# Optimization experiments

Hardware: AMD Instinct MI355X
Metric: run time of the kernel (lower is better)

The kernel has to match this reference:

```python
import jax, jax.numpy as jnp
import numpy as np
import math

B, S, HID = 2, 2048, 4096
H, HD = 32, HID // 32  # num_heads, head_dim


def setup_inputs() -> dict:
    key = jax.random.key(0)
    ks = jax.random.split(key, 7)
    hidden_states = jax.random.normal(ks[0], (B, S, HID), jnp.float32)
    residual = jax.random.normal(ks[1], (B, S, HID), jnp.float32)
    # BLOOM alibi: [B*H, 1, kv_len]; realistic slopes * positions
    slopes = jnp.asarray(2.0 ** (-8.0 * (np.arange(1, H + 1) / H)), jnp.float32)  # [H]
    alibi = (slopes[:, None] * jnp.arange(S, dtype=jnp.float32)[None, :])  # [H, S]
    alibi = jnp.broadcast_to(alibi[None], (B, H, S)).reshape(B * H, 1, S)
    # causal mask: True = masked (upper triangle)
    causal = ~jnp.tril(jnp.ones((S, S), bool))
    attention_mask = jnp.broadcast_to(causal[None, None], (B, 1, S, S))
    Wqkv = jax.random.normal(ks[2], (HID, 3 * HID), jnp.float32) * 0.02
    bqkv = jax.random.normal(ks[3], (3 * HID,), jnp.float32) * 0.02
    Wd = jax.random.normal(ks[4], (HID, HID), jnp.float32) * 0.02
    bd = jax.random.normal(ks[5], (HID,), jnp.float32) * 0.02
    return {"hidden_states": hidden_states, "residual": residual, "alibi": alibi,
            "attention_mask": attention_mask, "Wqkv": Wqkv, "bqkv": bqkv,
            "Wd": Wd, "bd": bd}


def reference(hidden_states, residual, alibi, attention_mask, Wqkv, bqkv, Wd, bd):
    b, s, _ = hidden_states.shape
    inv_norm = 1.0 / math.sqrt(HD)
    fused = hidden_states @ Wqkv + bqkv                       # [b,s,3*HID]
    fused = fused.reshape(b, s, H, 3, HD)
    q = jnp.transpose(fused[..., 0, :], (0, 2, 1, 3))         # [b,H,s,hd]
    k = jnp.transpose(fused[..., 1, :], (0, 2, 1, 3))
    v = jnp.transpose(fused[..., 2, :], (0, 2, 1, 3))
    # baddbmm: alibi + inv_norm * q @ k^T
    scores = jnp.einsum('bhqd,bhkd->bhqk', q, k) * inv_norm
    scores = scores + alibi.reshape(b, H, 1, s)               # broadcast over q
    neg = jnp.finfo(jnp.float32).min
    scores = jnp.where(attention_mask, neg, scores)
    probs = jax.nn.softmax(scores.astype(jnp.float32), axis=-1)
    ctx = jnp.einsum('bhqk,bhkd->bhqd', probs, v)             # [b,H,s,hd]
    ctx = jnp.transpose(ctx, (0, 2, 1, 3)).reshape(b, s, HID)
    out = ctx @ Wd + bd
    return residual + out
```

## Files before the change

### kernel.cpp

```cpp
#include <hip/hip_runtime.h>
#include <cstdint>
#include <cstddef>


typedef unsigned short u16;
typedef unsigned int u32;
typedef __bf16 bf16x8 __attribute__((ext_vector_type(8)));
typedef float f32x4 __attribute__((ext_vector_type(4)));
typedef u16 u16x4 __attribute__((ext_vector_type(4)));

#define LDS_AS(p) ((__attribute__((address_space(3))) u32*)(p))
#define GLB_AS(p) ((__attribute__((address_space(1))) u32*)(p))

__device__ __forceinline__ void load16(const void* g, void* l) {
  __builtin_amdgcn_global_load_lds(GLB_AS(g), LDS_AS(l), 16, 0, 0);
}

__device__ __forceinline__ u16 f2bf(float f) {
  union { float f; u32 u; } x; x.f = f;
  u32 r = x.u + 0x7fffu + ((x.u >> 16) & 1u);
  return (u16)(r >> 16);
}

__global__ __launch_bounds__(256) void cvt_bf16(const float* __restrict__ in,
                                                u16* __restrict__ out, int n) {
  int i = (blockIdx.x * 256 + threadIdx.x) * 4;
  if (i >= n) return;
  float4 v = *(const float4*)(in + i);
  u16x4 o = { f2bf(v.x), f2bf(v.y), f2bf(v.z), f2bf(v.w) };
  *(u16x4*)(out + i) = o;
}

__global__ __launch_bounds__(256) void cvt_transpose(const float* __restrict__ W,
                                                     u16* __restrict__ WT,
                                                     int K, int N) {
  __shared__ float tile[32][33];
  int n0 = blockIdx.x * 32, k0 = blockIdx.y * 32;
  int tx = threadIdx.x & 31, ty = threadIdx.x >> 5;
  for (int r = ty; r < 32; r += 8)
    tile[r][tx] = W[(size_t)(k0 + r) * N + n0 + tx];
  __syncthreads();
  for (int r = ty; r < 32; r += 8)
    WT[(size_t)(n0 + r) * K + k0 + tx] = f2bf(tile[tx][r]);
}

__global__ __launch_bounds__(256) void transpose_v(const u16* __restrict__ fused,
                                                   u16* __restrict__ vt) {
  __shared__ __align__(16) u16 tile[64][136];
  int st = blockIdx.x * 64, bh = blockIdx.y;
  int b = bh >> 5, h = bh & 31;
  int tx = threadIdx.x & 15, ty = threadIdx.x >> 4;
  for (int r = ty; r < 64; r += 16) {
    const u16* src = fused + (size_t)(b * 2048 + st + r) * 12288 + h * 384 + 256 + tx * 8;
    u16x4 a = *(const u16x4*)(src);
    u16x4 c = *(const u16x4*)(src + 4);
    *(u16x4*)&tile[r][tx * 8] = a;
    *(u16x4*)&tile[r][tx * 8 + 4] = c;
  }
  __syncthreads();
  for (int d = ty; d < 128; d += 16) {
    u16x4 o = { tile[tx * 4 + 0][d], tile[tx * 4 + 1][d],
                tile[tx * 4 + 2][d], tile[tx * 4 + 3][d] };
    *(u16x4*)(vt + ((size_t)bh * 128 + d) * 2048 + st + tx * 4) = o;
  }
}

template <int EPI>
__global__ __launch_bounds__(256) void gemm_bt(const u16* __restrict__ A,
                                               const u16* __restrict__ BT,
                                               const float* __restrict__ bias,
                                               const float* __restrict__ res,
                                               void* __restrict__ out,
                                               int M, int N, int K) {
  __shared__ __align__(16) u16 As[128 * 32];
  __shared__ __align__(16) u16 Bs[128 * 32];
  const int tid = threadIdx.x, wave = tid >> 6, lane = tid & 63;
  const int quad = lane >> 4, l16 = lane & 15;
  const int m0 = blockIdx.y * 128, n0 = blockIdx.x * 128;
  const int wm = (wave >> 1) * 64, wn = (wave & 1) * 64;

  const f32x4 fz = {0.f, 0.f, 0.f, 0.f};
  f32x4 acc[4][4];
  for (int i = 0; i < 4; ++i)
    for (int j = 0; j < 4; ++j) acc[i][j] = fz;

  const int i0 = wave * 2;
  const int t0 = i0 * 1024 + lane * 16;
  const int t1 = t0 + 1024;
  const int rA0 = t0 >> 6, cA0 = t0 & 63;
  const int rA1 = t1 >> 6, cA1 = t1 & 63;

  for (int k0 = 0; k0 < K; k0 += 32) {
    __syncthreads();
    load16((const char*)(A + (size_t)(m0 + rA0) * K + k0) + cA0, (char*)As + i0 * 1024);
    load16((const char*)(A + (size_t)(m0 + rA1) * K + k0) + cA1, (char*)As + i0 * 1024 + 1024);
    load16((const char*)(BT + (size_t)(n0 + rA0) * K + k0) + cA0, (char*)Bs + i0 * 1024);
    load16((const char*)(BT + (size_t)(n0 + rA1) * K + k0) + cA1, (char*)Bs + i0 * 1024 + 1024);
    __syncthreads();

    bf16x8 af[4], bfv[4];
    for (int i = 0; i < 4; ++i)
      af[i] = *(const bf16x8*)((const char*)As + ((wm + i * 16 + l16) * 32 + quad * 8) * 2);
    for (int j = 0; j < 4; ++j)
      bfv[j] = *(const bf16x8*)((const char*)Bs + ((wn + j * 16 + l16) * 32 + quad * 8) * 2);
    for (int i = 0; i < 4; ++i)
      for (int j = 0; j < 4; ++j)
        acc[i][j] = __builtin_amdgcn_mfma_f32_16x16x32_bf16(af[i], bfv[j], acc[i][j], 0, 0, 0);
  }

  for (int i = 0; i < 4; ++i) {
    int row = m0 + wm + i * 16 + quad * 4;
    for (int j = 0; j < 4; ++j) {
      int col = n0 + wn + j * 16 + l16;
      float bv = bias[col];
      for (int t = 0; t < 4; ++t) {
        float v = acc[i][j][t] + bv;
        size_t idx = (size_t)(row + t) * N + col;
        if (EPI == 1) {
          ((float*)out)[idx] = v + res[idx];
        } else {
          ((u16*)out)[idx] = f2bf(v);
        }
      }
    }
  }
}

__global__ __launch_bounds__(256) void flash_attn(const u16* __restrict__ fused,
                                                  const u16* __restrict__ vt,
                                                  const float* __restrict__ alibi,
                                                  u16* __restrict__ ctx) {
  __shared__ __align__(16) u16 Kbuf[2][64 * 128];
  __shared__ __align__(16) u16 Vbuf[128 * 64];
  __shared__ __align__(16) u16 Ps[64 * 72];

  const int tid = threadIdx.x, wave = tid >> 6, lane = tid & 63;
  const int quad = lane >> 4, l16 = lane & 15;
  const int qt = blockIdx.x, bh = blockIdx.y;
  const int b = bh >> 5, h = bh & 31;
  const int q0 = qt * 64;
  const float scale = 0.08838834764831845f;
  const f32x4 fz = {0.f, 0.f, 0.f, 0.f};

  const u16* srcQ[4];
  const u16* srcK[4];
  for (int j = 0; j < 4; ++j) {
    int inst = wave * 4 + j;
    int row = inst * 4 + quad;
    int cg = l16 ^ (row & 15);
    srcQ[j] = fused + (size_t)(b * 2048 + q0 + row) * 12288 + h * 384 + cg * 8;
    srcK[j] = fused + (size_t)(b * 2048 + row) * 12288 + h * 384 + 128 + cg * 8;
  }
  const u16* srcV[4];
  for (int j = 0; j < 4; ++j) {
    int inst = wave * 4 + j;
    int row = inst * 8 + (lane >> 3);
    int cg = (lane & 7) ^ (row & 7);
    srcV[j] = vt + ((size_t)bh * 128 + row) * 2048 + cg * 8;
  }

  for (int j = 0; j < 4; ++j) {
    int inst = wave * 4 + j;
    load16(srcQ[j], (char*)Kbuf[1] + inst * 1024);
    load16(srcK[j], (char*)Kbuf[0] + inst * 1024);
  }
  __syncthreads();

  bf16x8 qf[4];
  for (int kk = 0; kk < 4; ++kk) {
    int row = wave * 16 + l16;
    int cs = (kk * 4 + quad) ^ l16;
    qf[kk] = *(const bf16x8*)((const char*)Kbuf[1] + row * 256 + cs * 16);
  }
  __syncthreads();

  float m_st[4] = {-__builtin_inff(), -__builtin_inff(), -__builtin_inff(), -__builtin_inff()};
  float l_st[4] = {0.f, 0.f, 0.f, 0.f};
  f32x4 o_acc[8];
  for (int f = 0; f < 8; ++f) o_acc[f] = fz;

  const int nkv = qt + 1;
  for (int kvt = 0; kvt < nkv; ++kvt) {
    const int kv0 = kvt * 64;
    const int cur = kvt & 1;

    for (int j = 0; j < 4; ++j) {
      int inst = wave * 4 + j;
      load16(srcV[j] + kv0, (char*)Vbuf + inst * 1024);
    }
    if (kvt + 1 < nkv) {
      for (int j = 0; j < 4; ++j) {
        int inst = wave * 4 + j;
        load16(srcK[j] + (size_t)(kv0 + 64) * 12288, (char*)Kbuf[cur ^ 1] + inst * 1024);
      }
    }

    f32x4 sa[4];
    for (int j = 0; j < 4; ++j) sa[j] = fz;
    for (int kk = 0; kk < 4; ++kk) {
      for (int j = 0; j < 4; ++j) {
        int row = j * 16 + l16;
        int cs = (kk * 4 + quad) ^ l16;
        bf16x8 bv = *(const bf16x8*)((const char*)Kbuf[cur] + row * 256 + cs * 16);
        sa[j] = __builtin_amdgcn_mfma_f32_16x16x32_bf16(qf[kk], bv, sa[j], 0, 0, 0);
      }
    }

    float al[4];
    for (int j = 0; j < 4; ++j) al[j] = alibi[(size_t)bh * 2048 + kv0 + j * 16 + l16];
    float p[4][4];
    const bool diag = (kvt == qt);
    for (int j = 0; j < 4; ++j) {
      int kvg = kv0 + j * 16 + l16;
      for (int t = 0; t < 4; ++t) {
        float v = sa[j][t] * scale + al[j];
        if (diag) {
          int qg = q0 + wave * 16 + quad * 4 + t;
          if (kvg > qg) v = -__builtin_inff();
        }
        p[j][t] = v;
      }
    }

    float mnew[4], alpha[4];
    for (int t = 0; t < 4; ++t) {
      float mx = fmaxf(fmaxf(p[0][t], p[1][t]), fmaxf(p[2][t], p[3][t]));
      for (int off = 1; off < 16; off <<= 1) mx = fmaxf(mx, __shfl_xor(mx, off, 64));
      mnew[t] = fmaxf(m_st[t], mx);
      alpha[t] = __expf(m_st[t] - mnew[t]);
      m_st[t] = mnew[t];
      float rs = 0.f;
      for (int j = 0; j < 4; ++j) {
        p[j][t] = __expf(p[j][t] - mnew[t]);
        rs += p[j][t];
      }
      for (int off = 1; off < 16; off <<= 1) rs += __shfl_xor(rs, off, 64);
      l_st[t] = l_st[t] * alpha[t] + rs;
    }
    for (int f = 0; f < 8; ++f)
      for (int t = 0; t < 4; ++t) o_acc[f][t] *= alpha[t];

    for (int j = 0; j < 4; ++j)
      for (int t = 0; t < 4; ++t)
        Ps[(wave * 16 + quad * 4 + t) * 72 + j * 16 + l16] = f2bf(p[j][t]);

    __syncthreads();

    for (int kk = 0; kk < 2; ++kk) {
      bf16x8 a = *(const bf16x8*)((const char*)Ps + ((wave * 16 + l16) * 72 + kk * 32 + quad * 8) * 2);
      for (int f = 0; f < 8; ++f) {
        int row = f * 16 + l16;
        int cs = (kk * 4 + quad) ^ (l16 & 7);
        bf16x8 bv = *(const bf16x8*)((const char*)Vbuf + row * 128 + cs * 16);
        o_acc[f] = __builtin_amdgcn_mfma_f32_16x16x32_bf16(a, bv, o_acc[f], 0, 0, 0);
      }
    }

    __syncthreads();
  }

  float invl[4];
  for (int t = 0; t < 4; ++t) invl[t] = 1.0f / l_st[t];
  for (int f = 0; f < 8; ++f) {
    int d = h * 128 + f * 16 + l16;
    for (int t = 0; t < 4; ++t) {
      int row = b * 2048 + q0 + wave * 16 + quad * 4 + t;
      ctx[(size_t)row * 4096 + d] = f2bf(o_acc[f][t] * invl[t]);
    }
  }
}

extern "C" void kernel_launch(void* const* d_in, const int* in_sizes, int n_in,
                              void* d_out, int out_size, void* d_ws, size_t ws_size,
                              hipStream_t stream) {
  const float* hs    = (const float*)d_in[0];
  const float* resid = (const float*)d_in[1];
  const float* alibi = (const float*)d_in[2];
  const float* Wqkv  = (const float*)d_in[4];
  const float* bqkv  = (const float*)d_in[5];
  const float* Wd    = (const float*)d_in[6];
  const float* bd    = (const float*)d_in[7];

  char* ws = (char*)d_ws;
  u16* Abf   = (u16*)(ws);
  u16* W1T   = (u16*)(ws + (size_t)33554432);
  u16* fused = (u16*)(ws + (size_t)134217728);
  u16* vtb   = (u16*)(ws + (size_t)234881024);
  u16* ctx   = (u16*)(ws);
  u16* W2T   = (u16*)(ws + (size_t)33554432);

  cvt_bf16<<<16384, 256, 0, stream>>>(hs, Abf, 16777216);
  cvt_transpose<<<dim3(384, 128), 256, 0, stream>>>(Wqkv, W1T, 4096, 12288);
  gemm_bt<0><<<dim3(96, 32), 256, 0, stream>>>(Abf, W1T, bqkv, nullptr, fused, 4096, 12288, 4096);
  transpose_v<<<dim3(32, 64), 256, 0, stream>>>(fused, vtb);
  cvt_transpose<<<dim3(128, 128), 256, 0, stream>>>(Wd, W2T, 4096, 4096);
  flash_attn<<<dim3(32, 64), 256, 0, stream>>>(fused, vtb, alibi, ctx);
  gemm_bt<1><<<dim3(32, 32), 256, 0, stream>>>(ctx, W2T, bd, resid, d_out, 4096, 4096, 4096);
}
```

Measured before the change: 1.520 ms.

## Swizzle GEMM LDS tiles to avoid bank conflicts and swap block raster order

The GEMM's LDS layout is XOR-swizzled. Each global-to-LDS load lane fetches a permuted 16-byte column group, and the fragment reads use the matching swizzled offsets, so the row-strided bf16x8 reads should spread across banks. Per-thread load pointers and LDS offsets are now computed once, outside the k loop. The block raster order is also swapped so that consecutive blocks walk along M while sharing the same weight N-tile, which aims at better L2 reuse of the weight matrix.

Measured after the change: 1.537 ms. No clear change (+1.1%).

```diff
diff --git a/kernel.cpp b/kernel.cpp
--- a/kernel.cpp
+++ b/kernel.cpp
@@ -76,7 +76,7 @@
   __shared__ __align__(16) u16 Bs[128 * 32];
   const int tid = threadIdx.x, wave = tid >> 6, lane = tid & 63;
   const int quad = lane >> 4, l16 = lane & 15;
-  const int m0 = blockIdx.y * 128, n0 = blockIdx.x * 128;
+  const int m0 = blockIdx.x * 128, n0 = blockIdx.y * 128;
   const int wm = (wave >> 1) * 64, wn = (wave & 1) * 64;
 
   const f32x4 fz = {0.f, 0.f, 0.f, 0.f};
@@ -85,24 +85,38 @@
     for (int j = 0; j < 4; ++j) acc[i][j] = fz;
 
   const int i0 = wave * 2;
-  const int t0 = i0 * 1024 + lane * 16;
-  const int t1 = t0 + 1024;
-  const int rA0 = t0 >> 6, cA0 = t0 & 63;
-  const int rA1 = t1 >> 6, cA1 = t1 & 63;
+  const u16* pA[2];
+  const u16* pB[2];
+  int ldsOff[2];
+  for (int t = 0; t < 2; ++t) {
+    int inst = i0 + t;
+    int row = inst * 16 + (lane >> 2);
+    int cg = (lane & 3) ^ ((row >> 1) & 3);
+    pA[t] = A + (size_t)(m0 + row) * K + cg * 8;
+    pB[t] = BT + (size_t)(n0 + row) * K + cg * 8;
+    ldsOff[t] = inst * 1024;
+  }
+  int offA[4], offB[4];
+  for (int i = 0; i < 4; ++i) {
+    int rA = wm + i * 16 + l16;
+    offA[i] = rA * 64 + ((quad ^ ((rA >> 1) & 3)) * 16);
+    int rB = wn + i * 16 + l16;
+    offB[i] = rB * 64 + ((quad ^ ((rB >> 1) & 3)) * 16);
+  }
 
   for (int k0 = 0; k0 < K; k0 += 32) {
     __syncthreads();
-    load16((const char*)(A + (size_t)(m0 + rA0) * K + k0) + cA0, (char*)As + i0 * 1024);
-    load16((const char*)(A + (size_t)(m0 + rA1) * K + k0) + cA1, (char*)As + i0 * 1024 + 1024);
-    load16((const char*)(BT + (size_t)(n0 + rA0) * K + k0) + cA0, (char*)Bs + i0 * 1024);
-    load16((const char*)(BT + (size_t)(n0 + rA1) * K + k0) + cA1, (char*)Bs + i0 * 1024 + 1024);
+    load16(pA[0] + k0, (char*)As + ldsOff[0]);
+    load16(pA[1] + k0, (char*)As + ldsOff[1]);
+    load16(pB[0] + k0, (char*)Bs + ldsOff[0]);
+    load16(pB[1] + k0, (char*)Bs + ldsOff[1]);
     __syncthreads();
 
     bf16x8 af[4], bfv[4];
     for (int i = 0; i < 4; ++i)
-      af[i] = *(const bf16x8*)((const char*)As + ((wm + i * 16 + l16) * 32 + quad * 8) * 2);
+      af[i] = *(const bf16x8*)((const char*)As + offA[i]);
     for (int j = 0; j < 4; ++j)
-      bfv[j] = *(const bf16x8*)((const char*)Bs + ((wn + j * 16 + l16) * 32 + quad * 8) * 2);
+      bfv[j] = *(const bf16x8*)((const char*)Bs + offB[j]);
     for (int i = 0; i < 4; ++i)
       for (int j = 0; j < 4; ++j)
         acc[i][j] = __builtin_amdgcn_mfma_f32_16x16x32_bf16(af[i], bfv[j], acc[i][j], 0, 0, 0);
@@ -291,7 +305,7 @@
 
   cvt_bf16<<<16384, 256, 0, stream>>>(hs, Abf, 16777216);
   cvt_transpose<<<dim3(384, 128), 256, 0, stream>>>(Wqkv, W1T, 4096, 12288);
-  gemm_bt<0><<<dim3(96, 32), 256, 0, stream>>>(Abf, W1T, bqkv, nullptr, fused, 4096, 12288, 4096);
+  gemm_bt<0><<<dim3(32, 96), 256, 0, stream>>>(Abf, W1T, bqkv, nullptr, fused, 4096, 12288, 4096);
   transpose_v<<<dim3(32, 64), 256, 0, stream>>>(fused, vtb);
   cvt_transpose<<<dim3(128, 128), 256, 0, stream>>>(Wd, W2T, 4096, 4096);
   flash_attn<<<dim3(32, 64), 256, 0, stream>>>(fused, vtb, alibi, ctx);
```
